# Optimization experiments

Hardware: AMD Instinct MI355X
Metric: run time of the kernel (lower is better)

The kernel has to match this reference:

```python
import jax, jax.numpy as jnp
import numpy as np

K = 16          # neighbors per center (init arg K)
EPS = 1e-5      # layernorm epsilon


def _dcconv(pos, ch, W, b, n_in, n_out, resnet_in=None, Wres=None, bres=None):
    """KNN-gathered distance-contained conv.
    pos: [B, n_in, 3], ch: [B, n_in, Cin], W: [Cout, K, Cin].
    Selects n_out strided centers, gathers K nearest neighbors, convolves.
    """
    stride = n_in // n_out
    idx = jnp.arange(n_out) * stride                      # static center indices
    cpos = pos[:, idx]                                    # [B, n_out, 3]
    # squared pairwise distances centers -> all points: [B, n_out, n_in]
    d2 = jnp.sum((cpos[:, :, None, :] - pos[:, None, :, :]) ** 2, axis=-1)
    _, knn = jax.lax.top_k(-d2, K)                        # [B, n_out, K]
    gathered = jax.vmap(lambda c, i: c[i])(ch, knn)       # [B, n_out, K, Cin]
    out = jnp.einsum('bnkc,okc->bno', gathered, W) + b    # [B, n_out, Cout]
    if resnet_in is None:
        res = ch[:, idx] @ Wres + bres                    # project skip to Cout
    else:
        res = resnet_in[:, idx]                           # downsample carried skip
    return cpos, out, res


def _layernorm(x, g, b):
    mu = jnp.mean(x, axis=-1, keepdims=True)
    var = jnp.var(x, axis=-1, keepdims=True)
    return (x - mu) * jax.lax.rsqrt(var + EPS) * g + b


def setup_inputs() -> dict:
    key = jax.random.key(0)
    ks = jax.random.split(key, 8)
    B, N, Cin, Cout = 2, 8192, 64, 128
    s1 = (2.0 / (K * Cin)) ** 0.5
    s2 = (2.0 / (K * Cout)) ** 0.5
    return {
        'position_matrix': jax.random.normal(ks[0], (B, N, 3), jnp.float32),
        'channel_matrix': jax.random.normal(ks[1], (B, N, Cin), jnp.float32),
        'W1': jax.random.normal(ks[2], (Cout, K, Cin), jnp.float32) * s1,
        'b1': jnp.full((Cout,), 0.01, jnp.float32),
        'Wres': jax.random.normal(ks[3], (Cin, Cout), jnp.float32) * (2.0 / Cin) ** 0.5,
        'bres': jnp.full((Cout,), 0.01, jnp.float32),
        'W2': jax.random.normal(ks[4], (Cout, K, Cout), jnp.float32) * s2,
        'b2': jnp.full((Cout,), 0.01, jnp.float32),
        'g1': jnp.ones((Cout,), jnp.float32),
        'be1': jnp.full((Cout,), 0.01, jnp.float32),
        'g2': jnp.ones((Cout,), jnp.float32),
        'be2': jnp.full((Cout,), 0.01, jnp.float32),
        'n0': 8192, 'n1': 4096, 'n2': 2048,
    }


def reference(position_matrix, channel_matrix, W1, b1, Wres, bres, W2, b2,
              g1, be1, g2, be2, n0, n1, n2):
    pos, ch, res = _dcconv(position_matrix, channel_matrix, W1, b1, n0, n1,
                           None, Wres, bres)
    ch = jax.nn.silu(_layernorm(ch, g1, be1))   # dropout=identity (eval)
    pos, ch, res = _dcconv(pos, ch, W2, b2, n1, n2, resnet_in=res)
    ch = jax.nn.silu(_layernorm(ch, g2, be2))   # dropout=identity (eval)
    ch = ch + res                               # residual add
    return pos, ch
```

## Files before the change

### kernel.cpp

```cpp
#include <hip/hip_runtime.h>
#include <cstdint>
#include <cstddef>

using u16 = unsigned short;
using u32 = unsigned int;
using u64 = unsigned long long;

typedef short bf16x8 __attribute__((ext_vector_type(8)));
typedef float f32x4 __attribute__((ext_vector_type(4)));

constexpr int N0 = 8192;
constexpr int N1 = 4096;
constexpr int N2 = 2048;
constexpr int COUT = 128;
constexpr int KNB = 16;

__device__ __forceinline__ float bf2f(u16 v) { return __uint_as_float(((u32)v) << 16); }
__device__ __forceinline__ u16 f2bf(float f) {
    u32 u = __float_as_uint(f);
    return (u16)((u + 0x7fffu + ((u >> 16) & 1u)) >> 16);
}
__device__ __forceinline__ void cvt8(const float* __restrict__ src, u16* __restrict__ dst, int e) {
    float t0[8];
    *(float4*)t0 = *(const float4*)(src + e);
    *(float4*)(t0 + 4) = *(const float4*)(src + e + 4);
    u16 o[8];
#pragma unroll
    for (int q = 0; q < 8; ++q) o[q] = f2bf(t0[q]);
    *(uint4*)(dst + e) = *(uint4*)o;
}

__device__ __forceinline__ float dist2s(float cx, float cy, float cz,
                                        float px, float py, float pz) {
#pragma clang fp contract(off)
    float dx = cx - px;
    float dy = cy - py;
    float dz = cz - pz;
    float s = dx * dx;
    s = s + dy * dy;
    s = s + dz * dz;
    return s;
}

template <int CTRL>
__device__ __forceinline__ u64 dpp64(u64 v) {
    int lo = (int)(u32)v, hi = (int)(u32)(v >> 32);
    int plo = __builtin_amdgcn_update_dpp(0, lo, CTRL, 0xF, 0xF, true);
    int phi = __builtin_amdgcn_update_dpp(0, hi, CTRL, 0xF, 0xF, true);
    return (((u64)(u32)phi) << 32) | (u32)plo;
}
__device__ __forceinline__ u64 dpp_prev_u64(u64 v) { return dpp64<0x111>(v); }

__device__ __forceinline__ u32 rdlane(u32 v, int l) {
    return (u32)__builtin_amdgcn_readlane((int)v, l);
}

template <int PSTRIDE>
__device__ __forceinline__ void knn_scan(const float* __restrict__ P,
                                         int c0row, int c1row, int cnt,
                                         int lane, u64& rk0, u64& rk1) {
    const float* c0p = P + (size_t)c0row * PSTRIDE;
    const float* c1p = P + (size_t)c1row * PSTRIDE;
    float c0x = c0p[0], c0y = c0p[1], c0z = c0p[2];
    float c1x = c1p[0], c1y = c1p[1], c1z = c1p[2];

    u64 key0, key1;
    {
        const float* pp = P + (size_t)lane * PSTRIDE;
        float px = pp[0], py = pp[1], pz = pp[2];
        u64 k0 = (((u64)__float_as_uint(dist2s(c0x, c0y, c0z, px, py, pz))) << 32) | (u32)lane;
        u64 k1 = (((u64)__float_as_uint(dist2s(c1x, c1y, c1z, px, py, pz))) << 32) | (u32)lane;
#pragma unroll
        for (int kk = 2; kk <= 64; kk <<= 1)
#pragma unroll
            for (int jj = kk >> 1; jj > 0; jj >>= 1) {
                u64 o0, o1;
                if (jj == 1)      { o0 = dpp64<0xB1>(k0);  o1 = dpp64<0xB1>(k1); }
                else if (jj == 2) { o0 = dpp64<0x4E>(k0);  o1 = dpp64<0x4E>(k1); }
                else if (jj == 8) { o0 = dpp64<0x128>(k0); o1 = dpp64<0x128>(k1); }
                else              { o0 = __shfl_xor(k0, jj, 64); o1 = __shfl_xor(k1, jj, 64); }
                bool keepmin = (((lane & jj) == 0) == ((lane & kk) == 0));
                k0 = keepmin ? ((o0 < k0) ? o0 : k0) : ((o0 > k0) ? o0 : k0);
                k1 = keepmin ? ((o1 < k1) ? o1 : k1) : ((o1 > k1) ? o1 : k1);
            }
        key0 = k0; key1 = k1;
    }
    u32 cut0 = rdlane((u32)(key0 >> 32), 15);
    u32 cut1 = rdlane((u32)(key1 >> 32), 15);

    {
        const float* pp = P + (size_t)(64 + lane) * PSTRIDE;
        float px = pp[0], py = pp[1], pz = pp[2];
        u32 d0 = __float_as_uint(dist2s(c0x, c0y, c0z, px, py, pz));
        u32 d1 = __float_as_uint(dist2s(c1x, c1y, c1z, px, py, pz));
        u64 ball0 = __ballot(d0 <= cut0);
        u64 ball1 = __ballot(d1 <= cut1);
        while (ball0 | ball1) {
            if (ball0) {
                int src = __ffsll((unsigned long long)ball0) - 1;
                ball0 &= ball0 - 1;
                u64 nk = (((u64)rdlane(d0, src)) << 32) | (u32)(64 + src);
                u64 prev = dpp_prev_u64(key0);
                key0 = (nk < key0) ? ((nk < prev) ? prev : nk) : key0;
            }
            if (ball1) {
                int src = __ffsll((unsigned long long)ball1) - 1;
                ball1 &= ball1 - 1;
                u64 nk = (((u64)rdlane(d1, src)) << 32) | (u32)(64 + src);
                u64 prev = dpp_prev_u64(key1);
                key1 = (nk < key1) ? ((nk < prev) ? prev : nk) : key1;
            }
        }
        cut0 = rdlane((u32)(key0 >> 32), 15);
        cut1 = rdlane((u32)(key1 >> 32), 15);
    }

    constexpr int STEPF = 128 * PSTRIDE;
    int nstep = (cnt - 128) >> 7;
    const float* cur = P + (size_t)(128 + 2 * lane) * PSTRIDE;
    float ax = cur[0], ay = cur[1], az = cur[2];
    float bx = cur[PSTRIDE], by = cur[PSTRIDE + 1], bz = cur[PSTRIDE + 2];
    for (int s = 0; s < nstep; ++s) {
        float cax = ax, cay = ay, caz = az, cbx = bx, cby = by, cbz = bz;
        cur += STEPF;
        if (s + 1 < nstep) {
            ax = cur[0]; ay = cur[1]; az = cur[2];
            bx = cur[PSTRIDE]; by = cur[PSTRIDE + 1]; bz = cur[PSTRIDE + 2];
        }
        int sb = 128 + (s << 7);
        u32 da0 = __float_as_uint(dist2s(c0x, c0y, c0z, cax, cay, caz));
        u32 da1 = __float_as_uint(dist2s(c1x, c1y, c1z, cax, cay, caz));
        u32 db0 = __float_as_uint(dist2s(c0x, c0y, c0z, cbx, cby, cbz));
        u32 db1 = __float_as_uint(dist2s(c1x, c1y, c1z, cbx, cby, cbz));
        u64 ba0 = __ballot(da0 <= cut0);
        u64 bb0 = __ballot(db0 <= cut0);
        u64 ba1 = __ballot(da1 <= cut1);
        u64 bb1 = __ballot(db1 <= cut1);
        while (ba0 | bb0 | ba1 | bb1) {
            if (ba0) {
                int src = __ffsll((unsigned long long)ba0) - 1;
                ba0 &= ba0 - 1;
                u64 nk = (((u64)rdlane(da0, src)) << 32) | (u32)(sb + 2 * src);
                u64 prev = dpp_prev_u64(key0);
                key0 = (nk < key0) ? ((nk < prev) ? prev : nk) : key0;
            }
            if (ba1) {
                int src = __ffsll((unsigned long long)ba1) - 1;
                ba1 &= ba1 - 1;
                u64 nk = (((u64)rdlane(da1, src)) << 32) | (u32)(sb + 2 * src);
                u64 prev = dpp_prev_u64(key1);
                key1 = (nk < key1) ? ((nk < prev) ? prev : nk) : key1;
            }
            if (bb0) {
                int src = __ffsll((unsigned long long)bb0) - 1;
                bb0 &= bb0 - 1;
                u64 nk = (((u64)rdlane(db0, src)) << 32) | (u32)(sb + 2 * src + 1);
                u64 prev = dpp_prev_u64(key0);
                key0 = (nk < key0) ? ((nk < prev) ? prev : nk) : key0;
            }
            if (bb1) {
                int src = __ffsll((unsigned long long)bb1) - 1;
                bb1 &= bb1 - 1;
                u64 nk = (((u64)rdlane(db1, src)) << 32) | (u32)(sb + 2 * src + 1);
                u64 prev = dpp_prev_u64(key1);
                key1 = (nk < key1) ? ((nk < prev) ? prev : nk) : key1;
            }
        }
        cut0 = rdlane((u32)(key0 >> 32), 15);
        cut1 = rdlane((u32)(key1 >> 32), 15);
    }
    rk0 = key0; rk1 = key1;
}

__global__ __launch_bounds__(256)
void knn_prep_kernel(const float* __restrict__ pos0, const float* __restrict__ ch0,
                     const float* __restrict__ W1, const float* __restrict__ W2,
                     const float* __restrict__ Wres,
                     int* __restrict__ knn1,
                     u16* __restrict__ ch0b, u16* __restrict__ W1b,
                     u16* __restrict__ W2b, u16* __restrict__ Wresb,
                     float* __restrict__ pos_out) {
    int blk = blockIdx.x, tid = threadIdx.x;
    int w = tid >> 6, lane = tid & 63;
    if (blk < 1024) {
        int wave = blk * 4 + w;
        int batch = wave >> 11, pj = wave & 2047;
        const float* P = pos0 + (size_t)batch * N0 * 3;
        u64 key0, key1;
        knn_scan<3>(P, 4 * pj, 4 * pj + 2, N0, lane, key0, key1);
        if (lane < 16) {
            knn1[((size_t)(batch * N1 + 2 * pj)) * KNB + lane] = (int)(u32)key0;
            knn1[((size_t)(batch * N1 + 2 * pj + 1)) * KNB + lane] = (int)(u32)key1;
        }
    } else if (blk < 1536) {
        cvt8(ch0, ch0b, ((blk - 1024) * 256 + tid) * 8);
    } else if (blk < 1600) {
        cvt8(W1, W1b, ((blk - 1536) * 256 + tid) * 8);
    } else if (blk < 1728) {
        cvt8(W2, W2b, ((blk - 1600) * 256 + tid) * 8);
    } else if (blk < 1760) {
        int t = (blk - 1728) * 256 + tid;
        int o = t >> 6, c = t & 63;
        Wresb[o * 64 + c] = f2bf(Wres[(size_t)c * COUT + o]);
    } else {
        int t = (blk - 1760) * 256 + tid;
        int b = t >> 11, r = t & 2047;
        const float* s = pos0 + ((size_t)(b * N0 + r * 4)) * 3;
        float* d = pos_out + ((size_t)(b * N2 + r)) * 3;
        d[0] = s[0]; d[1] = s[1]; d[2] = s[2];
    }
}

__global__ __launch_bounds__(256)
void conv1_knn2_kernel(const u16* __restrict__ ch0b, const int* __restrict__ knn1,
                       const u16* __restrict__ W1b, const u16* __restrict__ Wresb,
                       const float* __restrict__ b1, const float* __restrict__ bres,
                       const float* __restrict__ g1, const float* __restrict__ be1,
                       u16* __restrict__ ch1b, u16* __restrict__ res1b,
                       const float* __restrict__ pos0, int* __restrict__ knn2) {
    __shared__ u16 As[2][16][72];
    __shared__ int knnr[16][16];
    __shared__ float red[16][4][2];
    __shared__ float cb[128], cg[128], cbe[128], cbr[128];

    int blk = blockIdx.x, tid = threadIdx.x;

    if (blk >= 512) {
        int w = tid >> 6, lane = tid & 63;
        int wave = (blk - 512) * 4 + w;
        int batch = wave >> 10, pj = wave & 1023;
        const float* P = pos0 + (size_t)batch * N0 * 3;
        u64 key0, key1;
        knn_scan<6>(P, 4 * pj, 4 * pj + 2, N1, lane, key0, key1);
        if (lane < 16) {
            knn2[((size_t)(batch * N2 + 2 * pj)) * KNB + lane] = (int)(u32)key0;
            knn2[((size_t)(batch * N2 + 2 * pj + 1)) * KNB + lane] = (int)(u32)key1;
        }
        return;
    }

    int b = blk >> 8, g = blk & 255;
    int jbase = g * 16;

    if (tid < 128) { cb[tid] = b1[tid]; cg[tid] = g1[tid]; cbe[tid] = be1[tid]; cbr[tid] = bres[tid]; }
    {
        int r = tid >> 4, k = tid & 15;
        knnr[r][k] = knn1[((size_t)(b * N1 + jbase + r)) * KNB + k];
    }
    __syncthreads();

    int w = tid >> 6, lane = tid & 63, quad = lane >> 4, l15 = lane & 15;
    int wcol = w * 32;
    int ar = tid >> 4, ap = tid & 15;

    f32x4 acc[2] = {{0,0,0,0},{0,0,0,0}};
    f32x4 racc[2] = {{0,0,0,0},{0,0,0,0}};

    const u16* w0base = W1b + (size_t)(wcol + l15) * 1024 + quad * 8;
    const u16* w1base = W1b + (size_t)(wcol + 16 + l15) * 1024 + quad * 8;

    uint2 aR = *((const uint2*)(ch0b + ((size_t)(b * N0 + knnr[ar][0])) * 64) + ap);
    uint4 wcur[4] = { *(const uint4*)w0base, *(const uint4*)(w0base + 32),
                      *(const uint4*)w1base, *(const uint4*)(w1base + 32) };

    int pb = 0;
    for (int kn = 0; kn < 17; ++kn) {
        *(uint2*)&As[pb][ar][ap * 4] = aR;
        __syncthreads();
        uint4 wnxt[4];
        if (kn < 16) {
            int nidx = (kn < 15) ? knnr[ar][kn + 1] : 2 * (jbase + ar);
            aR = *((const uint2*)(ch0b + ((size_t)(b * N0 + nidx)) * 64) + ap);
            if (kn < 15) {
                const u16* p0 = w0base + (kn + 1) * 64;
                const u16* p1 = w1base + (kn + 1) * 64;
                wnxt[0] = *(const uint4*)p0; wnxt[1] = *(const uint4*)(p0 + 32);
                wnxt[2] = *(const uint4*)p1; wnxt[3] = *(const uint4*)(p1 + 32);
            } else {
                const u16* p0 = Wresb + (size_t)(wcol + l15) * 64 + quad * 8;
                const u16* p1 = Wresb + (size_t)(wcol + 16 + l15) * 64 + quad * 8;
                wnxt[0] = *(const uint4*)p0; wnxt[1] = *(const uint4*)(p0 + 32);
                wnxt[2] = *(const uint4*)p1; wnxt[3] = *(const uint4*)(p1 + 32);
            }
        }
        if (kn < 16) {
#pragma unroll
            for (int ks = 0; ks < 2; ++ks) {
                bf16x8 af = *(const bf16x8*)&As[pb][l15][ks * 32 + quad * 8];
                acc[0] = __builtin_amdgcn_mfma_f32_16x16x32_bf16(af, *(const bf16x8*)&wcur[ks], acc[0], 0, 0, 0);
                acc[1] = __builtin_amdgcn_mfma_f32_16x16x32_bf16(af, *(const bf16x8*)&wcur[2 + ks], acc[1], 0, 0, 0);
            }
        } else {
#pragma unroll
            for (int ks = 0; ks < 2; ++ks) {
                bf16x8 af = *(const bf16x8*)&As[pb][l15][ks * 32 + quad * 8];
                racc[0] = __builtin_amdgcn_mfma_f32_16x16x32_bf16(af, *(const bf16x8*)&wcur[ks], racc[0], 0, 0, 0);
                racc[1] = __builtin_amdgcn_mfma_f32_16x16x32_bf16(af, *(const bf16x8*)&wcur[2 + ks], racc[1], 0, 0, 0);
            }
        }
        if (kn < 16) {
            wcur[0] = wnxt[0]; wcur[1] = wnxt[1]; wcur[2] = wnxt[2]; wcur[3] = wnxt[3];
        }
        pb ^= 1;
    }

    float x[2][4], s[4] = {0,0,0,0}, ss[4] = {0,0,0,0};
#pragma unroll
    for (int reg = 0; reg < 4; ++reg)
#pragma unroll
        for (int nt = 0; nt < 2; ++nt) {
            int col = wcol + nt * 16 + l15;
            float v = acc[nt][reg] + cb[col];
            x[nt][reg] = v;
            s[reg] += v; ss[reg] += v * v;
        }
#pragma unroll
    for (int m = 1; m < 16; m <<= 1)
#pragma unroll
        for (int reg = 0; reg < 4; ++reg) {
            s[reg] += __shfl_xor(s[reg], m, 64);
            ss[reg] += __shfl_xor(ss[reg], m, 64);
        }
    if (l15 == 0) {
#pragma unroll
        for (int reg = 0; reg < 4; ++reg) {
            red[quad * 4 + reg][w][0] = s[reg];
            red[quad * 4 + reg][w][1] = ss[reg];
        }
    }
    __syncthreads();
    float mu[4], rs[4];
#pragma unroll
    for (int reg = 0; reg < 4; ++reg) {
        int row = quad * 4 + reg;
        float S = red[row][0][0] + red[row][1][0] + red[row][2][0] + red[row][3][0];
        float SS = red[row][0][1] + red[row][1][1] + red[row][2][1] + red[row][3][1];
        mu[reg] = S * (1.f / 128.f);
        float var = fmaxf(SS * (1.f / 128.f) - mu[reg] * mu[reg], 0.f);
        rs[reg] = 1.f / sqrtf(var + 1e-5f);
    }
#pragma unroll
    for (int nt = 0; nt < 2; ++nt)
#pragma unroll
        for (int reg = 0; reg < 4; ++reg) {
            int col = wcol + nt * 16 + l15;
            int row = quad * 4 + reg;
            size_t off = ((size_t)(b * N1 + jbase + row)) * COUT + col;
            float y = (x[nt][reg] - mu[reg]) * rs[reg] * cg[col] + cbe[col];
            ch1b[off] = f2bf(y / (1.f + __expf(-y)));
            res1b[off] = f2bf(racc[nt][reg] + cbr[col]);
        }
}

__global__ __launch_bounds__(512)
void conv2_kernel(const u16* __restrict__ ch1b, const int* __restrict__ knn2,
                  const u16* __restrict__ W2b, const float* __restrict__ b2,
                  const float* __restrict__ g2, const float* __restrict__ be2,
                  const u16* __restrict__ res1b, float* __restrict__ ch_out) {
    __shared__ u16 As[2][16][136];
    __shared__ int knnr[16][16];
    __shared__ float red[16][8][2];
    __shared__ float cb[128], cg[128], cbe[128];

    int tid = threadIdx.x;
    int b = blockIdx.x >> 7, g = blockIdx.x & 127;
    int ibase = g * 16;

    if (tid < 128) { cb[tid] = b2[tid]; cg[tid] = g2[tid]; cbe[tid] = be2[tid]; }
    if (tid < 256) {
        int r = tid >> 4, k = tid & 15;
        knnr[r][k] = knn2[((size_t)(b * N2 + ibase + r)) * KNB + k];
    }
    __syncthreads();

    int w = tid >> 6, lane = tid & 63, quad = lane >> 4, l15 = lane & 15;
    int wcol = w * 16;
    int ar = tid >> 5, ap = tid & 31;

    f32x4 acc = {0, 0, 0, 0};

    const u16* wbase = W2b + (size_t)(wcol + l15) * 2048 + quad * 8;

    uint2 aR = *((const uint2*)(ch1b + ((size_t)(b * N1 + knnr[ar][0])) * COUT) + ap);
    uint4 wcur[4] = { *(const uint4*)wbase, *(const uint4*)(wbase + 32),
                      *(const uint4*)(wbase + 64), *(const uint4*)(wbase + 96) };

    int pb = 0;
    for (int kn = 0; kn < 16; ++kn) {
        *(uint2*)&As[pb][ar][ap * 4] = aR;
        __syncthreads();
        uint4 wnxt[4];
        if (kn < 15) {
            aR = *((const uint2*)(ch1b + ((size_t)(b * N1 + knnr[ar][kn + 1])) * COUT) + ap);
            const u16* p = wbase + (kn + 1) * 128;
            wnxt[0] = *(const uint4*)p;        wnxt[1] = *(const uint4*)(p + 32);
            wnxt[2] = *(const uint4*)(p + 64); wnxt[3] = *(const uint4*)(p + 96);
        }
#pragma unroll
        for (int ks = 0; ks < 4; ++ks) {
            bf16x8 af = *(const bf16x8*)&As[pb][l15][ks * 32 + quad * 8];
            acc = __builtin_amdgcn_mfma_f32_16x16x32_bf16(af, *(const bf16x8*)&wcur[ks], acc, 0, 0, 0);
        }
        if (kn < 15) {
            wcur[0] = wnxt[0]; wcur[1] = wnxt[1]; wcur[2] = wnxt[2]; wcur[3] = wnxt[3];
        }
        pb ^= 1;
    }

    float x[4], s[4], ss[4];
#pragma unroll
    for (int reg = 0; reg < 4; ++reg) {
        int col = wcol + l15;
        float v = acc[reg] + cb[col];
        x[reg] = v; s[reg] = v; ss[reg] = v * v;
    }
#pragma unroll
    for (int m = 1; m < 16; m <<= 1)
#pragma unroll
        for (int reg = 0; reg < 4; ++reg) {
            s[reg] += __shfl_xor(s[reg], m, 64);
            ss[reg] += __shfl_xor(ss[reg], m, 64);
        }
    if (l15 == 0) {
#pragma unroll
        for (int reg = 0; reg < 4; ++reg) {
            red[quad * 4 + reg][w][0] = s[reg];
            red[quad * 4 + reg][w][1] = ss[reg];
        }
    }
    __syncthreads();
#pragma unroll
    for (int reg = 0; reg < 4; ++reg) {
        int row = quad * 4 + reg;
        float S = 0.f, SS = 0.f;
#pragma unroll
        for (int t = 0; t < 8; ++t) { S += red[row][t][0]; SS += red[row][t][1]; }
        float mu = S * (1.f / 128.f);
        float var = fmaxf(SS * (1.f / 128.f) - mu * mu, 0.f);
        float rs = 1.f / sqrtf(var + 1e-5f);
        int col = wcol + l15;
        int i = ibase + row;
        float y = (x[reg] - mu) * rs * cg[col] + cbe[col];
        float sl = y / (1.f + __expf(-y));
        float rv = bf2f(res1b[((size_t)(b * N1 + 2 * i)) * COUT + col]);
        ch_out[((size_t)(b * N2 + i)) * COUT + col] = sl + rv;
    }
}

extern "C" void kernel_launch(void* const* d_in, const int* in_sizes, int n_in,
                              void* d_out, int out_size, void* d_ws, size_t ws_size,
                              hipStream_t stream) {
    const float* pos0 = (const float*)d_in[0];
    const float* ch0  = (const float*)d_in[1];
    const float* W1   = (const float*)d_in[2];
    const float* b1   = (const float*)d_in[3];
    const float* Wres = (const float*)d_in[4];
    const float* bres = (const float*)d_in[5];
    const float* W2   = (const float*)d_in[6];
    const float* b2   = (const float*)d_in[7];
    const float* g1   = (const float*)d_in[8];
    const float* be1  = (const float*)d_in[9];
    const float* g2   = (const float*)d_in[10];
    const float* be2  = (const float*)d_in[11];
    float* out = (float*)d_out;

    char* ws = (char*)d_ws;
    int*  knn1  = (int*)(ws);
    int*  knn2  = (int*)(ws + 524288);
    u16*  ch0b  = (u16*)(ws + 786432);
    u16*  W1b   = (u16*)(ws + 2883584);
    u16*  W2b   = (u16*)(ws + 3145728);
    u16*  Wresb = (u16*)(ws + 3670016);
    u16*  ch1b  = (u16*)(ws + 3686400);
    u16*  res1b = (u16*)(ws + 5783552);

    float* pos_out = out;
    float* ch_out  = out + 12288;

    knn_prep_kernel<<<1776, 256, 0, stream>>>(pos0, ch0, W1, W2, Wres,
                                              knn1, ch0b, W1b, W2b, Wresb, pos_out);
    conv1_knn2_kernel<<<1024, 256, 0, stream>>>(ch0b, knn1, W1b, Wresb, b1, bres, g1, be1,
                                                ch1b, res1b, pos0, knn2);
    conv2_kernel<<<256, 512, 0, stream>>>(ch1b, knn2, W2b, b2, g2, be2, res1b, ch_out);
}
```

Baseline: 189.1 us.

## Split KNN scan across two waves per center pair and merge top-16 via bitonic

Each KNN center pair is now scanned by two waves, each covering half of the point set. The two partial top-16 lists are exchanged through shared memory and combined with a 32-element bitonic merge. This halves the serial scan length per wave and doubles the number of waves, so latency-bound scans should finish sooner. The cost is more blocks, an added __syncthreads and merge step, and a weaker pruning cutoff in each half-scan, which may admit more candidate insertions.

```diff
diff --git a/kernel.cpp b/kernel.cpp
--- a/kernel.cpp
+++ b/kernel.cpp
@@ -56,20 +56,16 @@
 }
 
 template <int PSTRIDE>
-__device__ __forceinline__ void knn_scan(const float* __restrict__ P,
-                                         int c0row, int c1row, int cnt,
+__device__ __forceinline__ void knn_scan(const float* __restrict__ P, int ibase, int cnt,
+                                         float c0x, float c0y, float c0z,
+                                         float c1x, float c1y, float c1z,
                                          int lane, u64& rk0, u64& rk1) {
-    const float* c0p = P + (size_t)c0row * PSTRIDE;
-    const float* c1p = P + (size_t)c1row * PSTRIDE;
-    float c0x = c0p[0], c0y = c0p[1], c0z = c0p[2];
-    float c1x = c1p[0], c1y = c1p[1], c1z = c1p[2];
-
     u64 key0, key1;
     {
         const float* pp = P + (size_t)lane * PSTRIDE;
         float px = pp[0], py = pp[1], pz = pp[2];
-        u64 k0 = (((u64)__float_as_uint(dist2s(c0x, c0y, c0z, px, py, pz))) << 32) | (u32)lane;
-        u64 k1 = (((u64)__float_as_uint(dist2s(c1x, c1y, c1z, px, py, pz))) << 32) | (u32)lane;
+        u64 k0 = (((u64)__float_as_uint(dist2s(c0x, c0y, c0z, px, py, pz))) << 32) | (u32)(ibase + lane);
+        u64 k1 = (((u64)__float_as_uint(dist2s(c1x, c1y, c1z, px, py, pz))) << 32) | (u32)(ibase + lane);
 #pragma unroll
         for (int kk = 2; kk <= 64; kk <<= 1)
 #pragma unroll
@@ -99,14 +95,14 @@
             if (ball0) {
                 int src = __ffsll((unsigned long long)ball0) - 1;
                 ball0 &= ball0 - 1;
-                u64 nk = (((u64)rdlane(d0, src)) << 32) | (u32)(64 + src);
+                u64 nk = (((u64)rdlane(d0, src)) << 32) | (u32)(ibase + 64 + src);
                 u64 prev = dpp_prev_u64(key0);
                 key0 = (nk < key0) ? ((nk < prev) ? prev : nk) : key0;
             }
             if (ball1) {
                 int src = __ffsll((unsigned long long)ball1) - 1;
                 ball1 &= ball1 - 1;
-                u64 nk = (((u64)rdlane(d1, src)) << 32) | (u32)(64 + src);
+                u64 nk = (((u64)rdlane(d1, src)) << 32) | (u32)(ibase + 64 + src);
                 u64 prev = dpp_prev_u64(key1);
                 key1 = (nk < key1) ? ((nk < prev) ? prev : nk) : key1;
             }
@@ -127,7 +123,7 @@
             ax = cur[0]; ay = cur[1]; az = cur[2];
             bx = cur[PSTRIDE]; by = cur[PSTRIDE + 1]; bz = cur[PSTRIDE + 2];
         }
-        int sb = 128 + (s << 7);
+        int sb = ibase + 128 + (s << 7);
         u32 da0 = __float_as_uint(dist2s(c0x, c0y, c0z, cax, cay, caz));
         u32 da1 = __float_as_uint(dist2s(c1x, c1y, c1z, cax, cay, caz));
         u32 db0 = __float_as_uint(dist2s(c0x, c0y, c0z, cbx, cby, cbz));
@@ -172,6 +168,19 @@
     rk0 = key0; rk1 = key1;
 }
 
+__device__ __forceinline__ u64 bitonic_merge32(u64 own, const u64* __restrict__ partner, int lane) {
+    u64 k;
+    if (lane < 16)      k = own;
+    else if (lane < 32) k = partner[31 - lane];
+    else                k = ~0ull;
+#pragma unroll
+    for (int j = 16; j > 0; j >>= 1) {
+        u64 o = __shfl_xor(k, j, 64);
+        k = ((lane & j) == 0) ? ((o < k) ? o : k) : ((o > k) ? o : k);
+    }
+    return k;
+}
+
 __global__ __launch_bounds__(256)
 void knn_prep_kernel(const float* __restrict__ pos0, const float* __restrict__ ch0,
                      const float* __restrict__ W1, const float* __restrict__ W2,
@@ -180,30 +189,38 @@
                      u16* __restrict__ ch0b, u16* __restrict__ W1b,
                      u16* __restrict__ W2b, u16* __restrict__ Wresb,
                      float* __restrict__ pos_out) {
+    __shared__ u64 mbuf[4][2][16];
     int blk = blockIdx.x, tid = threadIdx.x;
     int w = tid >> 6, lane = tid & 63;
-    if (blk < 1024) {
-        int wave = blk * 4 + w;
-        int batch = wave >> 11, pj = wave & 2047;
+    if (blk < 2048) {
+        int pairwave = blk * 2 + (w >> 1);
+        int h = w & 1;
+        int batch = pairwave >> 11, pj = pairwave & 2047;
         const float* P = pos0 + (size_t)batch * N0 * 3;
+        const float* c0p = P + (size_t)(4 * pj) * 3;
+        const float* c1p = P + (size_t)(4 * pj + 2) * 3;
+        constexpr int HALF = 4096;
         u64 key0, key1;
-        knn_scan<3>(P, 4 * pj, 4 * pj + 2, N0, lane, key0, key1);
-        if (lane < 16) {
-            knn1[((size_t)(batch * N1 + 2 * pj)) * KNB + lane] = (int)(u32)key0;
-            knn1[((size_t)(batch * N1 + 2 * pj + 1)) * KNB + lane] = (int)(u32)key1;
-        }
-    } else if (blk < 1536) {
-        cvt8(ch0, ch0b, ((blk - 1024) * 256 + tid) * 8);
-    } else if (blk < 1600) {
-        cvt8(W1, W1b, ((blk - 1536) * 256 + tid) * 8);
-    } else if (blk < 1728) {
-        cvt8(W2, W2b, ((blk - 1600) * 256 + tid) * 8);
-    } else if (blk < 1760) {
-        int t = (blk - 1728) * 256 + tid;
+        knn_scan<3>(P + (size_t)h * HALF * 3, h * HALF, HALF,
+                    c0p[0], c0p[1], c0p[2], c1p[0], c1p[1], c1p[2], lane, key0, key1);
+        if (lane < 16) { mbuf[w][0][lane] = key0; mbuf[w][1][lane] = key1; }
+        __syncthreads();
+        u64 own = h ? key1 : key0;
+        u64 merged = bitonic_merge32(own, &mbuf[w ^ 1][h][0], lane);
+        if (lane < 16)
+            knn1[((size_t)(batch * N1 + 2 * pj + h)) * KNB + lane] = (int)(u32)merged;
+    } else if (blk < 2560) {
+        cvt8(ch0, ch0b, ((blk - 2048) * 256 + tid) * 8);
+    } else if (blk < 2624) {
+        cvt8(W1, W1b, ((blk - 2560) * 256 + tid) * 8);
+    } else if (blk < 2752) {
+        cvt8(W2, W2b, ((blk - 2624) * 256 + tid) * 8);
+    } else if (blk < 2784) {
+        int t = (blk - 2752) * 256 + tid;
         int o = t >> 6, c = t & 63;
         Wresb[o * 64 + c] = f2bf(Wres[(size_t)c * COUT + o]);
     } else {
-        int t = (blk - 1760) * 256 + tid;
+        int t = (blk - 2784) * 256 + tid;
         int b = t >> 11, r = t & 2047;
         const float* s = pos0 + ((size_t)(b * N0 + r * 4)) * 3;
         float* d = pos_out + ((size_t)(b * N2 + r)) * 3;
@@ -222,20 +239,29 @@
     __shared__ int knnr[16][16];
     __shared__ float red[16][4][2];
     __shared__ float cb[128], cg[128], cbe[128], cbr[128];
+    __shared__ u64 mbuf[4][2][16];
 
     int blk = blockIdx.x, tid = threadIdx.x;
 
     if (blk >= 512) {
         int w = tid >> 6, lane = tid & 63;
-        int wave = (blk - 512) * 4 + w;
-        int batch = wave >> 10, pj = wave & 1023;
+        int t = blk - 512;
+        int pairwave = t * 2 + (w >> 1);
+        int h = w & 1;
+        int batch = pairwave >> 10, pj = pairwave & 1023;
         const float* P = pos0 + (size_t)batch * N0 * 3;
+        const float* c0p = P + (size_t)(4 * pj) * 6;
+        const float* c1p = P + (size_t)(4 * pj + 2) * 6;
+        constexpr int HALF = 2048;
         u64 key0, key1;
-        knn_scan<6>(P, 4 * pj, 4 * pj + 2, N1, lane, key0, key1);
-        if (lane < 16) {
-            knn2[((size_t)(batch * N2 + 2 * pj)) * KNB + lane] = (int)(u32)key0;
-            knn2[((size_t)(batch * N2 + 2 * pj + 1)) * KNB + lane] = (int)(u32)key1;
-        }
+        knn_scan<6>(P + (size_t)h * HALF * 6, h * HALF, HALF,
+                    c0p[0], c0p[1], c0p[2], c1p[0], c1p[1], c1p[2], lane, key0, key1);
+        if (lane < 16) { mbuf[w][0][lane] = key0; mbuf[w][1][lane] = key1; }
+        __syncthreads();
+        u64 own = h ? key1 : key0;
+        u64 merged = bitonic_merge32(own, &mbuf[w ^ 1][h][0], lane);
+        if (lane < 16)
+            knn2[((size_t)(batch * N2 + 2 * pj + h)) * KNB + lane] = (int)(u32)merged;
         return;
     }
 
@@ -477,9 +503,9 @@
     float* pos_out = out;
     float* ch_out  = out + 12288;
 
-    knn_prep_kernel<<<1776, 256, 0, stream>>>(pos0, ch0, W1, W2, Wres,
+    knn_prep_kernel<<<2800, 256, 0, stream>>>(pos0, ch0, W1, W2, Wres,
                                               knn1, ch0b, W1b, W2b, Wresb, pos_out);
-    conv1_knn2_kernel<<<1024, 256, 0, stream>>>(ch0b, knn1, W1b, Wresb, b1, bres, g1, be1,
+    conv1_knn2_kernel<<<1536, 256, 0, stream>>>(ch0b, knn1, W1b, Wresb, b1, bres, g1, be1,
                                                 ch1b, res1b, pos0, knn2);
     conv2_kernel<<<256, 512, 0, stream>>>(ch1b, knn2, W2b, b2, g2, be2, res1b, ch_out);
 }
```

Result: slower. 204.8 us (+8.3%).
